# Performance work log

Hardware: AMD Instinct MI355X
Metric: run time of the kernel (lower is better)

Reference implementation:

```python
import jax, jax.numpy as jnp
import numpy as np

L, N, D = 1024, 64, 1024  # seq_len, batch, d_model (= hidden)


def setup_inputs() -> dict:
    key = jax.random.key(0)
    k1, k2, k3 = jax.random.split(key, 3)
    x = jax.random.normal(k1, (L, N, D), dtype=jnp.float32)
    # flax OptimizedLSTMCell params: input kernel (no bias), recurrent kernel + bias,
    # gates packed as [i, f, g, o] along last dim.
    Wi = jax.random.normal(k2, (D, 4 * D), dtype=jnp.float32) / np.float32(np.sqrt(D))
    Wh = jax.random.normal(k3, (D, 4 * D), dtype=jnp.float32) / np.float32(np.sqrt(D))
    b = jnp.zeros((4 * D,), dtype=jnp.float32)
    return {"x": x, "Wi": Wi, "Wh": Wh, "b": b}


def reference(x, Wi, Wh, b):
    # x: [L, N, D]; scan LSTM cell over time axis 0 (matches nn.scan in_axes=0).
    d = Wh.shape[0]
    n = x.shape[1]
    # Input projections have no carry dependency: batch them in one big GEMM.
    xW = jnp.einsum('lnd,df->lnf', x, Wi)  # [L, N, 4D]

    def step(carry, xw_t):
        c, h = carry
        y = xw_t + h @ Wh + b  # [N, 4D]
        i, f, g, o = jnp.split(y, 4, axis=-1)
        i = jax.nn.sigmoid(i)
        f = jax.nn.sigmoid(f)
        g = jnp.tanh(g)
        o = jax.nn.sigmoid(o)
        c_new = f * c + i * g
        h_new = o * jnp.tanh(c_new)
        return (c_new, h_new), h_new

    c0 = jnp.zeros((n, d), dtype=x.dtype)
    h0 = jnp.zeros((n, d), dtype=x.dtype)
    _, hs = jax.lax.scan(step, (c0, h0), xW)
    return hs  # [L, N, D]
```

## Files before the change

### kernel.cpp

```cpp
#include <hip/hip_runtime.h>
#include <stdint.h>

#define LSEQ 1024
#define NB   64
#define DM   1024
#define FOURD 4096

typedef float f32x4 __attribute__((ext_vector_type(4)));
typedef short short8_t __attribute__((ext_vector_type(8)));
typedef __bf16 bf16x8 __attribute__((ext_vector_type(8)));

__device__ __forceinline__ unsigned short f2bf(float f) {
    unsigned int u = __builtin_bit_cast(unsigned int, f);
    u += 0x7fffu + ((u >> 16) & 1u);
    return (unsigned short)(u >> 16);
}

__device__ __forceinline__ f32x4 mfma16(short8_t a, short8_t b, f32x4 c) {
    return __builtin_amdgcn_mfma_f32_16x16x32_bf16(
        __builtin_bit_cast(bf16x8, a), __builtin_bit_cast(bf16x8, b), c, 0, 0, 0);
}

__global__ void init_ws_kernel(unsigned int* __restrict__ p, int n) {
    int i = blockIdx.x * blockDim.x + threadIdx.x;
    int stride = gridDim.x * blockDim.x;
    for (; i < n; i += stride) p[i] = 0u;
}

__global__ void convert_x_kernel(const float4* __restrict__ src, uint4* __restrict__ dst) {
    size_t i = (size_t)blockIdx.x * blockDim.x + threadIdx.x;
    float4 a = src[2 * i];
    float4 b = src[2 * i + 1];
    uint4 r;
    r.x = (unsigned)f2bf(a.x) | ((unsigned)f2bf(a.y) << 16);
    r.y = (unsigned)f2bf(a.z) | ((unsigned)f2bf(a.w) << 16);
    r.z = (unsigned)f2bf(b.x) | ((unsigned)f2bf(b.y) << 16);
    r.w = (unsigned)f2bf(b.z) | ((unsigned)f2bf(b.w) << 16);
    dst[i] = r;
}

__global__ void transpose_wi_kernel(const float* __restrict__ Wi,
                                    unsigned short* __restrict__ wt) {
    __shared__ float tl[32][33];
    const int bx = blockIdx.x & 127;
    const int by = blockIdx.x >> 7;
    const int c = threadIdx.x & 31;
    const int r = threadIdx.x >> 5;
    const int k0 = by * 32, c0 = bx * 32;
    #pragma unroll
    for (int j = 0; j < 4; ++j)
        tl[r + j * 8][c] = Wi[(size_t)(k0 + r + j * 8) * 4096 + c0 + c];
    __syncthreads();
    #pragma unroll
    for (int j = 0; j < 4; ++j)
        wt[(size_t)(c0 + r + j * 8) * 1024 + k0 + c] = f2bf(tl[c][r + j * 8]);
}

__global__ void prep_wh_kernel(const float* __restrict__ Wh,
                               unsigned short* __restrict__ whp) {
    const int fid = blockIdx.x * 256 + threadIdx.x;
    const int lane = fid & 63;
    const int kk = (fid >> 6) & 7;
    const int q  = (fid >> 9) & 3;
    const int ks = (fid >> 11) & 3;
    const int ug = fid >> 13;
    const int k0 = (ks << 8) + (kk << 5) + ((lane >> 4) << 3);
    const int col = (q << 10) + (ug << 4) + (lane & 15);
    short8_t v;
    #pragma unroll
    for (int j = 0; j < 8; ++j)
        v[j] = (short)f2bf(Wh[(size_t)(k0 + j) * FOURD + col]);
    *(short8_t*)(whp + ((size_t)fid << 3)) = v;
}

__device__ __forceinline__ void gload_lds16(const void* g, void* l) {
    __builtin_amdgcn_global_load_lds(
        (const __attribute__((address_space(1))) void*)g,
        (__attribute__((address_space(3))) void*)l, 16, 0, 0);
}

#define GSTAGE(dstbuf, src, kt)                                                    \
    { _Pragma("unroll")                                                            \
      for (int j_ = 0; j_ < 4; ++j_) {                                             \
        const int rr_ = ((wv << 2) + j_) * 8 + (lane >> 3);                        \
        const int lc_ = (lane & 7) ^ (rr_ & 7);                                    \
        gload_lds16((src) + (size_t)rr_ * 1024 + (kt) * 64 + lc_ * 8,              \
                    (dstbuf) + ((wv << 2) + j_) * 512);                            \
      } }

__global__ __launch_bounds__(256, 2)
void gemm_xw_kernel(const unsigned short* __restrict__ A,
                    const unsigned short* __restrict__ Bt,
                    float* __restrict__ C)
{
    __shared__ unsigned short sA[2][8192];
    __shared__ unsigned short sB[2][8192];
    const int tid = threadIdx.x;
    const int lane = tid & 63, wv = tid >> 6;
    const int wr = wv >> 1, wc = wv & 1;
    const int bx = blockIdx.x & 31;
    const int by = blockIdx.x >> 5;
    const unsigned short* Ab = A + (size_t)by * 128 * 1024;
    const unsigned short* Bb = Bt + (size_t)bx * 128 * 1024;
    const int kseg = lane >> 4, la = lane & 15;

    f32x4 acc[4][4];
    #pragma unroll
    for (int i = 0; i < 4; ++i)
        #pragma unroll
        for (int j = 0; j < 4; ++j) acc[i][j] = (f32x4){0.f, 0.f, 0.f, 0.f};

    GSTAGE(sA[0], Ab, 0)
    GSTAGE(sB[0], Bb, 0)
    asm volatile("s_waitcnt vmcnt(0)" ::: "memory");
    __syncthreads();

    int cur = 0;
    for (int kt = 0; kt < 16; ++kt) {
        if (kt < 15) {
            GSTAGE(sA[cur ^ 1], Ab, kt + 1)
            GSTAGE(sB[cur ^ 1], Bb, kt + 1)
        }
        short8_t af[4][2], bf[4][2];
        #pragma unroll
        for (int mt = 0; mt < 4; ++mt) {
            const int row = (wr << 6) + (mt << 4) + la;
            #pragma unroll
            for (int kk = 0; kk < 2; ++kk)
                af[mt][kk] = *(const short8_t*)((const char*)&sA[cur][0]
                    + row * 128 + ((((kk << 2) + kseg) ^ (row & 7)) << 4));
        }
        #pragma unroll
        for (int nt = 0; nt < 4; ++nt) {
            const int row = (wc << 6) + (nt << 4) + la;
            #pragma unroll
            for (int kk = 0; kk < 2; ++kk)
                bf[nt][kk] = *(const short8_t*)((const char*)&sB[cur][0]
                    + row * 128 + ((((kk << 2) + kseg) ^ (row & 7)) << 4));
        }
        #pragma unroll
        for (int kk = 0; kk < 2; ++kk)
            #pragma unroll
            for (int mt = 0; mt < 4; ++mt)
                #pragma unroll
                for (int nt = 0; nt < 4; ++nt)
                    acc[mt][nt] = mfma16(af[mt][kk], bf[nt][kk], acc[mt][nt]);
        asm volatile("s_waitcnt vmcnt(0)" ::: "memory");
        __syncthreads();
        cur ^= 1;
    }

    #pragma unroll
    for (int mt = 0; mt < 4; ++mt)
        #pragma unroll
        for (int nt = 0; nt < 4; ++nt)
            #pragma unroll
            for (int j = 0; j < 4; ++j)
                C[(size_t)(by * 128 + (wr << 6) + (mt << 4) + (kseg << 2) + j) * 4096
                  + bx * 128 + (wc << 6) + (nt << 4) + la] = acc[mt][nt][j];
}

#define HL(arr, i, OFFS)                                                        \
    asm volatile("global_load_dwordx4 %0, %1, off offset:" OFFS " sc0 sc1"      \
                 : "=v"(arr[i]) : "v"(hap) : "memory")
#define WAITV(NSTR)                                          \
    asm volatile("s_waitcnt vmcnt(" NSTR ")" ::: "memory");  \
    __builtin_amdgcn_sched_barrier(0)
#define HM(arr, i, kk) {                                        \
    short8_t b = *(const short8_t*)(bph + (kk) * 1024);         \
    if ((kk) & 1) acc1 = mfma16(arr[i], b, acc1);               \
    else          acc0 = mfma16(arr[i], b, acc0); }

__global__ __launch_bounds__(256, 1)
void lstm_scan_kernel(const unsigned short* __restrict__ whp,
                      const float* __restrict__ bias,
                      const float* __restrict__ xwc,
                      float* __restrict__ cbuf,
                      unsigned short* __restrict__ hbuf,
                      unsigned int* __restrict__ flags,
                      float* __restrict__ out,
                      int t0, int t1)
{
    __shared__ float plds[4][4][16][20];
    const int tid = threadIdx.x;
    const int wg = blockIdx.x;
    const int rg = wg >> 6, ug = wg & 63;
    const int r0 = rg << 4, U0 = ug << 4;
    const int lane = tid & 63, ks = tid >> 6;
    const int la = lane & 15, kseg = lane >> 4;

    short8_t B[4][8];
    const unsigned short* wb = whp + (((size_t)(ug << 2) + ks) << 14);
    #pragma unroll
    for (int q = 0; q < 4; ++q)
        #pragma unroll
        for (int kk = 0; kk < 8; ++kk)
            B[q][kk] = *(const short8_t*)(wb + ((((q << 3) + kk) << 9) + (lane << 3)));

    const int er = tid >> 4, eu = tid & 15;
    const float bI = bias[U0 + eu], bF = bias[1024 + U0 + eu],
                bG = bias[2048 + U0 + eu], bO = bias[3072 + U0 + eu];
    float cst = cbuf[(size_t)(r0 + er) * DM + U0 + eu];
    unsigned int* myflag = flags + (rg << 6) + ug;
    const unsigned int* gfp = flags + (rg << 6);

    for (int t = t0; t < t1; ++t) {
        const int lt = t - t0;
        const float* xp = xwc + ((size_t)(lt * NB) + r0 + er) * FOURD + U0 + eu;
        float x0 = xp[0], x1 = xp[1024], x2 = xp[2048], x3 = xp[3072];
        asm volatile("" :: "v"(x0), "v"(x1), "v"(x2), "v"(x3));

        if (t && tid < 64) {
            while (true) {
                unsigned int f = __hip_atomic_load(gfp + tid, __ATOMIC_RELAXED,
                                                  __HIP_MEMORY_SCOPE_AGENT);
                if (__all((int)(f >= (unsigned)t))) break;
                __builtin_amdgcn_s_sleep(1);
            }
        }
        __syncthreads();

        const unsigned short* hap = hbuf + (size_t)((t & 1) ^ 1) * (NB * DM)
                                  + (size_t)(r0 + la) * DM + (ks << 8) + (kseg << 3);
        short8_t Af[8];
        HL(Af, 0, "0");   HL(Af, 1, "64");  HL(Af, 2, "128"); HL(Af, 3, "192");
        HL(Af, 4, "256"); HL(Af, 5, "320"); HL(Af, 6, "384"); HL(Af, 7, "448");

        f32x4 acc[4];
        #pragma unroll
        for (int q = 0; q < 4; ++q) acc[q] = (f32x4){0.f, 0.f, 0.f, 0.f};

        WAITV("4");
        #pragma unroll
        for (int kk = 0; kk < 4; ++kk)
            #pragma unroll
            for (int q = 0; q < 4; ++q)
                acc[q] = mfma16(Af[kk], B[q][kk], acc[q]);
        WAITV("0");
        #pragma unroll
        for (int kk = 4; kk < 8; ++kk)
            #pragma unroll
            for (int q = 0; q < 4; ++q)
                acc[q] = mfma16(Af[kk], B[q][kk], acc[q]);

        #pragma unroll
        for (int q = 0; q < 4; ++q)
            *(f32x4*)&plds[ks][q][la][kseg << 2] = acc[q];
        __syncthreads();

        float vi = x0 + bI + plds[0][0][eu][er] + plds[1][0][eu][er]
                           + plds[2][0][eu][er] + plds[3][0][eu][er];
        float vf = x1 + bF + plds[0][1][eu][er] + plds[1][1][eu][er]
                           + plds[2][1][eu][er] + plds[3][1][eu][er];
        float vg = x2 + bG + plds[0][2][eu][er] + plds[1][2][eu][er]
                           + plds[2][2][eu][er] + plds[3][2][eu][er];
        float vo = x3 + bO + plds[0][3][eu][er] + plds[1][3][eu][er]
                           + plds[2][3][eu][er] + plds[3][3][eu][er];
        float gi = 1.0f / (1.0f + __expf(-vi));
        float gF = 1.0f / (1.0f + __expf(-vf));
        float gg = 1.0f - 2.0f / (__expf(2.0f * vg) + 1.0f);
        float go = 1.0f / (1.0f + __expf(-vo));
        cst = gF * cst + gi * gg;
        float hv = go * (1.0f - 2.0f / (__expf(2.0f * cst) + 1.0f));

        float hn = __shfl_xor(hv, 1);
        if (!(eu & 1)) {
            const int n = r0 + er;
            const int d = U0 + eu;
            unsigned int hp = (unsigned)f2bf(hv) | ((unsigned)f2bf(hn) << 16);
            __hip_atomic_store((unsigned int*)(hbuf + (size_t)(t & 1) * (NB * DM)
                                               + (size_t)n * DM + d),
                               hp, __ATOMIC_RELAXED, __HIP_MEMORY_SCOPE_AGENT);
            *(float2*)(out + ((size_t)(t * NB) + n) * DM + d) = make_float2(hv, hn);
        }
        asm volatile("s_waitcnt vmcnt(0)" ::: "memory");
        __syncthreads();
        if (tid == 0)
            __hip_atomic_store(myflag, (unsigned)(t + 1), __ATOMIC_RELAXED,
                               __HIP_MEMORY_SCOPE_AGENT);
    }
    cbuf[(size_t)(r0 + er) * DM + U0 + eu] = cst;
}

template <int XB>
__global__ __launch_bounds__(256)
void lstm_kernel(const float* __restrict__ x,
                 const float* __restrict__ Wi,
                 const float* __restrict__ Wh,
                 const float* __restrict__ bias,
                 const unsigned short* __restrict__ xb,
                 unsigned short* __restrict__ hbuf,
                 unsigned int* __restrict__ flags,
                 float* __restrict__ out)
{
    __shared__ short Wlds[65536];
    __shared__ float ylds[32 * 33];
    __shared__ float blds[32];

    const int tid  = threadIdx.x;
    const int wgid = blockIdx.x;
    const int g    = wgid >> 7;
    const int ug   = wgid & 127;
    const int U0   = ug << 3;
    const int rowbase = g << 5;

    {
        const int c    = tid & 31;
        const int ct_  = c >> 4;
        const int lb   = c & 15;
        const int gcol = ((c >> 3) << 10) + U0 + (c & 7);
        for (int k = tid >> 5; k < 1024; k += 8) {
            const int lane_ = lb | (((k >> 3) & 3) << 4);
            const int sidx  = (ct_ * 32 + (k >> 5)) * 512 + lane_ * 8 + (k & 7);
            Wlds[sidx]         = (short)f2bf(Wi[(size_t)k * FOURD + gcol]);
            Wlds[sidx + 32768] = (short)f2bf(Wh[(size_t)k * FOURD + gcol]);
        }
        if (tid < 32) blds[tid] = bias[((tid >> 3) << 10) + U0 + (tid & 7)];
    }
    __syncthreads();

    const int lane = tid & 63;
    const int wv   = tid >> 6;
    const int rt   = wv >> 1;
    const int ct   = wv & 1;
    const int arow = rowbase + (rt << 4) + (lane & 15);
    const int kseg = (lane >> 4) << 3;
    const char* bpx = (const char*)Wlds + ct * 32768 + lane * 16;
    const char* bph = (const char*)Wlds + 65536 + ct * 32768 + lane * 16;

    const int er = tid >> 3;
    const int eu = tid & 7;
    const float bI = blds[eu], bF = blds[8 + eu], bG = blds[16 + eu], bO = blds[24 + eu];
    float cstate = 0.0f;
    unsigned int* gflags = flags + (g << 7);

    for (int t = 0; t < LSEQ; ++t) {
        f32x4 acc0 = {0.f, 0.f, 0.f, 0.f};
        f32x4 acc1 = {0.f, 0.f, 0.f, 0.f};

        if (XB) {
            const unsigned short* ap = xb + ((size_t)t * NB + arow) * DM + kseg;
            #pragma unroll 8
            for (int kk = 0; kk < 32; ++kk) {
                short8_t a = *(const short8_t*)(ap + kk * 32);
                short8_t b = *(const short8_t*)(bpx + kk * 1024);
                if (kk & 1) acc1 = mfma16(a, b, acc1);
                else        acc0 = mfma16(a, b, acc0);
            }
        } else {
            const float* ap = x + ((size_t)t * NB + arow) * DM + kseg;
            #pragma unroll 4
            for (int kk = 0; kk < 32; ++kk) {
                float4 lo = *(const float4*)(ap + kk * 32);
                float4 hi = *(const float4*)(ap + kk * 32 + 4);
                short8_t a;
                a[0] = (short)f2bf(lo.x); a[1] = (short)f2bf(lo.y);
                a[2] = (short)f2bf(lo.z); a[3] = (short)f2bf(lo.w);
                a[4] = (short)f2bf(hi.x); a[5] = (short)f2bf(hi.y);
                a[6] = (short)f2bf(hi.z); a[7] = (short)f2bf(hi.w);
                short8_t b = *(const short8_t*)(bpx + kk * 1024);
                if (kk & 1) acc1 = mfma16(a, b, acc1);
                else        acc0 = mfma16(a, b, acc0);
            }
        }

        if (t && wv == 0) {
            const unsigned int* fp = gflags + (lane << 1);
            while (true) {
                unsigned int f0 = __hip_atomic_load(fp,     __ATOMIC_RELAXED, __HIP_MEMORY_SCOPE_AGENT);
                unsigned int f1 = __hip_atomic_load(fp + 1, __ATOMIC_RELAXED, __HIP_MEMORY_SCOPE_AGENT);
                int ok = (f0 >= (unsigned)t) && (f1 >= (unsigned)t);
                if (__all(ok)) break;
                __builtin_amdgcn_s_sleep(1);
            }
        }
        __syncthreads();

        {
            const unsigned short* hap =
                hbuf + (size_t)((t & 1) ^ 1) * (NB * DM) + (size_t)arow * DM + kseg;
            short8_t A0[8], A1[8];
            HL(A0,0,"0");    HL(A0,1,"64");   HL(A0,2,"128");  HL(A0,3,"192");
            HL(A0,4,"256");  HL(A0,5,"320");  HL(A0,6,"384");  HL(A0,7,"448");
            HL(A1,0,"512");  HL(A1,1,"576");  HL(A1,2,"640");  HL(A1,3,"704");
            HL(A1,4,"768");  HL(A1,5,"832");  HL(A1,6,"896");  HL(A1,7,"960");
            WAITV("8");
            HM(A0,0,0)  HM(A0,1,1)  HM(A0,2,2)  HM(A0,3,3)
            HM(A0,4,4)  HM(A0,5,5)  HM(A0,6,6)  HM(A0,7,7)
            HL(A0,0,"1024"); HL(A0,1,"1088"); HL(A0,2,"1152"); HL(A0,3,"1216");
            HL(A0,4,"1280"); HL(A0,5,"1344"); HL(A0,6,"1408"); HL(A0,7,"1472");
            WAITV("8");
            HM(A1,0,8)  HM(A1,1,9)  HM(A1,2,10) HM(A1,3,11)
            HM(A1,4,12) HM(A1,5,13) HM(A1,6,14) HM(A1,7,15)
            HL(A1,0,"1536"); HL(A1,1,"1600"); HL(A1,2,"1664"); HL(A1,3,"1728");
            HL(A1,4,"1792"); HL(A1,5,"1856"); HL(A1,6,"1920"); HL(A1,7,"1984");
            WAITV("8");
            HM(A0,0,16) HM(A0,1,17) HM(A0,2,18) HM(A0,3,19)
            HM(A0,4,20) HM(A0,5,21) HM(A0,6,22) HM(A0,7,23)
            WAITV("0");
            HM(A1,0,24) HM(A1,1,25) HM(A1,2,26) HM(A1,3,27)
            HM(A1,4,28) HM(A1,5,29) HM(A1,6,30) HM(A1,7,31)
        }

        {
            f32x4 acc = acc0 + acc1;
            const int rr0 = (rt << 4) + ((lane >> 4) << 2);
            const int c0 = (ct << 4) + (lane & 15);
            #pragma unroll
            for (int j = 0; j < 4; ++j) ylds[(rr0 + j) * 33 + c0] = acc[j];
        }
        __syncthreads();

        {
            const float* yr = ylds + er * 33;
            float vi = yr[eu]      + bI;
            float vf = yr[8 + eu]  + bF;
            float vg = yr[16 + eu] + bG;
            float vo = yr[24 + eu] + bO;
            float gi = 1.0f / (1.0f + __expf(-vi));
            float gF = 1.0f / (1.0f + __expf(-vf));
            float gg = 1.0f - 2.0f / (__expf(2.0f * vg) + 1.0f);
            float go = 1.0f / (1.0f + __expf(-vo));
            cstate = gF * cstate + gi * gg;
            float hv = go * (1.0f - 2.0f / (__expf(2.0f * cstate) + 1.0f));
            float hvn = __shfl_down(hv, 1);
            if ((tid & 1) == 0) {
                const int n = rowbase + er;
                const int d = U0 + eu;
                unsigned int hp = (unsigned)f2bf(hv) | ((unsigned)f2bf(hvn) << 16);
                unsigned int* hw = (unsigned int*)(hbuf + (size_t)(t & 1) * (NB * DM)
                                                   + (size_t)n * DM + d);
                __hip_atomic_store(hw, hp, __ATOMIC_RELAXED, __HIP_MEMORY_SCOPE_AGENT);
                *(float2*)(out + ((size_t)t * NB + n) * DM + d) = make_float2(hv, hvn);
            }
        }
        asm volatile("s_waitcnt vmcnt(0)" ::: "memory");
        __syncthreads();

        if (tid == 0) {
            __hip_atomic_store(gflags + ug, (unsigned)(t + 1),
                               __ATOMIC_RELAXED, __HIP_MEMORY_SCOPE_AGENT);
            asm volatile("s_waitcnt vmcnt(0)" ::: "memory");
        }
    }
}

extern "C" void kernel_launch(void* const* d_in, const int* in_sizes, int n_in,
                              void* d_out, int out_size, void* d_ws, size_t ws_size,
                              hipStream_t stream) {
    (void)in_sizes; (void)n_in; (void)out_size;
    const float* x  = (const float*)d_in[0];
    const float* Wi = (const float*)d_in[1];
    const float* Wh = (const float*)d_in[2];
    const float* b  = (const float*)d_in[3];
    float* out = (float*)d_out;

    char* ws = (char*)d_ws;
    const size_t OFF_HB  = 4096;
    const size_t OFF_CB  = OFF_HB + 262144;
    const size_t OFF_WT  = OFF_CB + 262144;
    const size_t OFF_WHP = OFF_WT + 8388608ull;
    const size_t OFF_XBC = OFF_WHP + 8388608ull;

    unsigned int*   flags = (unsigned int*)ws;
    unsigned short* hbuf  = (unsigned short*)(ws + OFF_HB);
    float*          cbuf  = (float*)(ws + OFF_CB);

    int CH = 0;
    const int cands[4] = {512, 256, 128, 64};
    for (int i = 0; i < 4; ++i) {
        size_t need = OFF_XBC + (size_t)cands[i] * (131072ull + 1048576ull);
        if (ws_size >= need) { CH = cands[i]; break; }
    }

    init_ws_kernel<<<64, 256, 0, stream>>>((unsigned int*)ws, 132096);

    if (CH) {
        unsigned short* wibt = (unsigned short*)(ws + OFF_WT);
        unsigned short* whp  = (unsigned short*)(ws + OFF_WHP);
        unsigned short* xbc  = (unsigned short*)(ws + OFF_XBC);
        float*          xwc  = (float*)(ws + OFF_XBC + (size_t)CH * 131072ull);

        transpose_wi_kernel<<<4096, 256, 0, stream>>>(Wi, wibt);
        prep_wh_kernel<<<2048, 256, 0, stream>>>(Wh, whp);

        const int nch = LSEQ / CH;
        for (int ci = 0; ci < nch; ++ci) {
            const int t0 = ci * CH;
            convert_x_kernel<<<CH * 32, 256, 0, stream>>>(
                (const float4*)(x + (size_t)t0 * NB * DM), (uint4*)xbc);
            gemm_xw_kernel<<<CH * 16, 256, 0, stream>>>(xbc, wibt, xwc);
            lstm_scan_kernel<<<256, 256, 0, stream>>>(whp, b, xwc, cbuf, hbuf,
                                                      flags, out, t0, t0 + CH);
        }
    } else if (ws_size >= 266240ull + 134217728ull) {
        unsigned short* xb = (unsigned short*)(ws + 266240);
        convert_x_kernel<<<32768, 256, 0, stream>>>((const float4*)x, (uint4*)xb);
        lstm_kernel<1><<<256, 256, 0, stream>>>(x, Wi, Wh, b, xb, hbuf, flags, out);
    } else {
        lstm_kernel<0><<<256, 256, 0, stream>>>(x, Wi, Wh, b, (const unsigned short*)ws,
                                                hbuf, flags, out);
    }
}
```

Baseline: 4.340 ms.

## Use per-wave flags and drop end-of-step barrier in LSTM scan

Each wave now publishes its own progress flag after its h stores drain, so the trailing __syncthreads and the single-thread flag store go away. Consumers poll four flags per lane with one uncached dwordx4 load and no sleep, and the output store moves after the flag release so it no longer delays the signal. The XB fallback path is removed. The risks are heavier spin traffic on the flags and getting memory ordering right with raw asm stores.

```diff
diff --git a/kernel.cpp b/kernel.cpp
--- a/kernel.cpp
+++ b/kernel.cpp
@@ -9,6 +9,7 @@
 typedef float f32x4 __attribute__((ext_vector_type(4)));
 typedef short short8_t __attribute__((ext_vector_type(8)));
 typedef __bf16 bf16x8 __attribute__((ext_vector_type(8)));
+typedef unsigned int uint4v __attribute__((ext_vector_type(4)));
 
 __device__ __forceinline__ unsigned short f2bf(float f) {
     unsigned int u = __builtin_bit_cast(unsigned int, f);
@@ -166,10 +167,11 @@
 #define WAITV(NSTR)                                          \
     asm volatile("s_waitcnt vmcnt(" NSTR ")" ::: "memory");  \
     __builtin_amdgcn_sched_barrier(0)
-#define HM(arr, i, kk) {                                        \
-    short8_t b = *(const short8_t*)(bph + (kk) * 1024);         \
-    if ((kk) & 1) acc1 = mfma16(arr[i], b, acc1);               \
-    else          acc0 = mfma16(arr[i], b, acc0); }
+#define WAITL()                                              \
+    asm volatile("s_waitcnt lgkmcnt(0)" ::: "memory")
+#define BARRIER()                                            \
+    __builtin_amdgcn_s_barrier();                            \
+    asm volatile("" ::: "memory")
 
 __global__ __launch_bounds__(256, 1)
 void lstm_scan_kernel(const unsigned short* __restrict__ whp,
@@ -201,24 +203,26 @@
     const float bI = bias[U0 + eu], bF = bias[1024 + U0 + eu],
                 bG = bias[2048 + U0 + eu], bO = bias[3072 + U0 + eu];
     float cst = cbuf[(size_t)(r0 + er) * DM + U0 + eu];
-    unsigned int* myflag = flags + (rg << 6) + ug;
-    const unsigned int* gfp = flags + (rg << 6);
+    unsigned int* myflag = flags + (((rg << 6) + ug) << 2) + ks;
+    const unsigned int* pfp = flags + (rg << 8) + (tid << 2);
 
     for (int t = t0; t < t1; ++t) {
         const int lt = t - t0;
         const float* xp = xwc + ((size_t)(lt * NB) + r0 + er) * FOURD + U0 + eu;
         float x0 = xp[0], x1 = xp[1024], x2 = xp[2048], x3 = xp[3072];
-        asm volatile("" :: "v"(x0), "v"(x1), "v"(x2), "v"(x3));
 
         if (t && tid < 64) {
             while (true) {
-                unsigned int f = __hip_atomic_load(gfp + tid, __ATOMIC_RELAXED,
-                                                  __HIP_MEMORY_SCOPE_AGENT);
-                if (__all((int)(f >= (unsigned)t))) break;
-                __builtin_amdgcn_s_sleep(1);
+                uint4v f;
+                asm volatile("global_load_dwordx4 %0, %1, off sc0 sc1\n\t"
+                             "s_waitcnt vmcnt(0)"
+                             : "=v"(f) : "v"(pfp) : "memory");
+                int ok = (f[0] >= (unsigned)t) && (f[1] >= (unsigned)t) &&
+                         (f[2] >= (unsigned)t) && (f[3] >= (unsigned)t);
+                if (__all(ok)) break;
             }
         }
-        __syncthreads();
+        BARRIER();
 
         const unsigned short* hap = hbuf + (size_t)((t & 1) ^ 1) * (NB * DM)
                                   + (size_t)(r0 + la) * DM + (ks << 8) + (kseg << 3);
@@ -246,7 +250,8 @@
         #pragma unroll
         for (int q = 0; q < 4; ++q)
             *(f32x4*)&plds[ks][q][la][kseg << 2] = acc[q];
-        __syncthreads();
+        WAITL();
+        BARRIER();
 
         float vi = x0 + bI + plds[0][0][eu][er] + plds[1][0][eu][er]
                            + plds[2][0][eu][er] + plds[3][0][eu][er];
@@ -265,33 +270,38 @@
 
         float hn = __shfl_xor(hv, 1);
         if (!(eu & 1)) {
-            const int n = r0 + er;
-            const int d = U0 + eu;
             unsigned int hp = (unsigned)f2bf(hv) | ((unsigned)f2bf(hn) << 16);
-            __hip_atomic_store((unsigned int*)(hbuf + (size_t)(t & 1) * (NB * DM)
-                                               + (size_t)n * DM + d),
-                               hp, __ATOMIC_RELAXED, __HIP_MEMORY_SCOPE_AGENT);
-            *(float2*)(out + ((size_t)(t * NB) + n) * DM + d) = make_float2(hv, hn);
-        }
-        asm volatile("s_waitcnt vmcnt(0)" ::: "memory");
-        __syncthreads();
-        if (tid == 0)
-            __hip_atomic_store(myflag, (unsigned)(t + 1), __ATOMIC_RELAXED,
-                               __HIP_MEMORY_SCOPE_AGENT);
+            unsigned int* hw = (unsigned int*)(hbuf + (size_t)(t & 1) * (NB * DM)
+                                               + (size_t)(r0 + er) * DM + U0 + eu);
+            asm volatile("global_store_dword %0, %1, off sc0 sc1"
+                         :: "v"(hw), "v"(hp) : "memory");
+        }
+        WAITV("0");
+        if ((tid & 63) == 0) {
+            unsigned int tv = (unsigned)(t + 1);
+            asm volatile("global_store_dword %0, %1, off sc0 sc1"
+                         :: "v"(myflag), "v"(tv) : "memory");
+        }
+        if (!(eu & 1))
+            *(float2*)(out + ((size_t)(t * NB) + r0 + er) * DM + U0 + eu)
+                = make_float2(hv, hn);
     }
     cbuf[(size_t)(r0 + er) * DM + U0 + eu] = cst;
 }
 
-template <int XB>
+#define HM(arr, i, kk) {                                        \
+    short8_t b = *(const short8_t*)(bph + (kk) * 1024);         \
+    if ((kk) & 1) acc1 = mfma16(arr[i], b, acc1);               \
+    else          acc0 = mfma16(arr[i], b, acc0); }
+
 __global__ __launch_bounds__(256)
-void lstm_kernel(const float* __restrict__ x,
-                 const float* __restrict__ Wi,
-                 const float* __restrict__ Wh,
-                 const float* __restrict__ bias,
-                 const unsigned short* __restrict__ xb,
-                 unsigned short* __restrict__ hbuf,
-                 unsigned int* __restrict__ flags,
-                 float* __restrict__ out)
+void lstm_fallback_kernel(const float* __restrict__ x,
+                          const float* __restrict__ Wi,
+                          const float* __restrict__ Wh,
+                          const float* __restrict__ bias,
+                          unsigned short* __restrict__ hbuf,
+                          unsigned int* __restrict__ flags,
+                          float* __restrict__ out)
 {
     __shared__ short Wlds[65536];
     __shared__ float ylds[32 * 33];
@@ -338,16 +348,7 @@
         f32x4 acc0 = {0.f, 0.f, 0.f, 0.f};
         f32x4 acc1 = {0.f, 0.f, 0.f, 0.f};
 
-        if (XB) {
-            const unsigned short* ap = xb + ((size_t)t * NB + arow) * DM + kseg;
-            #pragma unroll 8
-            for (int kk = 0; kk < 32; ++kk) {
-                short8_t a = *(const short8_t*)(ap + kk * 32);
-                short8_t b = *(const short8_t*)(bpx + kk * 1024);
-                if (kk & 1) acc1 = mfma16(a, b, acc1);
-                else        acc0 = mfma16(a, b, acc0);
-            }
-        } else {
+        {
             const float* ap = x + ((size_t)t * NB + arow) * DM + kseg;
             #pragma unroll 4
             for (int kk = 0; kk < 32; ++kk) {
@@ -493,12 +494,8 @@
             lstm_scan_kernel<<<256, 256, 0, stream>>>(whp, b, xwc, cbuf, hbuf,
                                                       flags, out, t0, t0 + CH);
         }
-    } else if (ws_size >= 266240ull + 134217728ull) {
-        unsigned short* xb = (unsigned short*)(ws + 266240);
-        convert_x_kernel<<<32768, 256, 0, stream>>>((const float4*)x, (uint4*)xb);
-        lstm_kernel<1><<<256, 256, 0, stream>>>(x, Wi, Wh, b, xb, hbuf, flags, out);
     } else {
-        lstm_kernel<0><<<256, 256, 0, stream>>>(x, Wi, Wh, b, (const unsigned short*)ws,
-                                                hbuf, flags, out);
+        lstm_fallback_kernel<<<256, 256, 0, stream>>>(x, Wi, Wh, b, hbuf,
+                                                      flags, out);
     }
 }
```

Result: slower. 6.843 ms (+57.7%).
